# Performance work log

Measured on AMD Instinct MI355X. Metric: run time of the kernel, lower is better.

The kernel has to match this reference:

```python
import jax, jax.numpy as jnp
import numpy as np

HEADS = 4
DIM_HEAD = 128
DIM = 128
INNER = HEADS * DIM_HEAD  # 512
MAX_POS = 100
SCALE = DIM_HEAD ** -0.5


def setup_inputs() -> dict:
    key = jax.random.key(0)
    ks = jax.random.split(key, 8)
    b, h, w = 2, 48, 64
    fmap1 = jax.random.normal(ks[0], (b, DIM, h, w), jnp.float32)
    fmap2 = jax.random.normal(ks[1], (b, DIM, h, w), jnp.float32)
    Wqk = jax.random.normal(ks[2], (2 * INNER, DIM), jnp.float32) * 0.05
    Wv = jax.random.normal(ks[3], (INNER, DIM), jnp.float32) * 0.05
    rel_h = jax.random.normal(ks[4], (2 * MAX_POS - 1, DIM_HEAD), jnp.float32) * 0.05
    rel_w = jax.random.normal(ks[5], (2 * MAX_POS - 1, DIM_HEAD), jnp.float32) * 0.05
    Wp = jax.random.normal(ks[6], (DIM, INNER), jnp.float32) * 0.05
    gamma = jnp.full((1,), 0.1, jnp.float32)  # nonzero so the attn path is active
    return {"fmap1": fmap1, "fmap2": fmap2, "Wqk": Wqk, "Wv": Wv,
            "rel_h": rel_h, "rel_w": rel_w, "Wp": Wp, "gamma": gamma}


def _aggregate(fmap, Wqk, Wv, rel_h, rel_w, Wp, gamma):
    b, c, H, W = fmap.shape
    # 1x1 conv = channel matmul
    qk = jnp.einsum('oc,bchw->bohw', Wqk, fmap)
    q = qk[:, :INNER] * SCALE  # k chunk unused (position-only similarity)
    # b (n d) h w -> b n h w d
    q = q.reshape(b, HEADS, DIM_HEAD, H, W).transpose(0, 1, 3, 4, 2)
    v = jnp.einsum('oc,bchw->bohw', Wv, fmap)
    v = v.reshape(b, HEADS, DIM_HEAD, H, W).transpose(0, 1, 3, 4, 2).reshape(b, HEADS, H * W, DIM_HEAD)
    # relative position similarity (RelPosEmb)
    idx_h = jnp.arange(H)[:, None] - jnp.arange(H)[None, :] + (MAX_POS - 1)  # (H,H)
    idx_w = jnp.arange(W)[:, None] - jnp.arange(W)[None, :] + (MAX_POS - 1)  # (W,W)
    He = rel_h[idx_h]  # (x,u,d)
    We = rel_w[idx_w]  # (y,v,d)
    hs = jnp.einsum('bnxyd,xud->bnxyu', q, He)  # (b,n,x,y,u)
    ws = jnp.einsum('bnxyd,yvd->bnxyv', q, We)  # (b,n,x,y,v)
    sim = hs[..., :, None] + ws[..., None, :]   # (b,n,x,y,u,v)
    sim = sim.reshape(b, HEADS, H * W, H * W)
    attn = jax.nn.softmax(sim, axis=-1)
    out = jnp.einsum('bnij,bnjd->bnid', attn, v)  # (b,n,hw,d)
    out = out.reshape(b, HEADS, H, W, DIM_HEAD).transpose(0, 1, 4, 2, 3).reshape(b, INNER, H, W)
    out = jnp.einsum('oc,bchw->bohw', Wp, out)  # project (dim != inner_dim)
    return fmap + gamma[0] * out


def reference(fmap1, fmap2, Wqk, Wv, rel_h, rel_w, Wp, gamma):
    out1 = _aggregate(fmap1, Wqk, Wv, rel_h, rel_w, Wp, gamma)
    out2 = _aggregate(fmap2, Wqk, Wv, rel_h, rel_w, Wp, gamma)
    return (out1, out2)
```

## Files before the change

### kernel.cpp

```cpp
#include <hip/hip_runtime.h>
#include <cstdint>
#include <cstddef>

typedef short bf16x8 __attribute__((ext_vector_type(8)));
typedef float f32x4 __attribute__((ext_vector_type(4)));

#define HH 48
#define WW 64
#define HWSZ 3072
#define SCALE_Q 0.08838834764831845f

__device__ __forceinline__ float b2f(unsigned short u) {
    union { unsigned int i; float f; } c; c.i = ((unsigned int)u) << 16; return c.f;
}
__device__ __forceinline__ unsigned short f2b(float f) {
    union { float f; unsigned int i; } c; c.f = f;
    unsigned int r = (c.i + 0x7fffu + ((c.i >> 16) & 1u)) >> 16;
    return (unsigned short)r;
}

__global__ __launch_bounds__(256) void k_transpose(const float* __restrict__ f0,
                                                   const float* __restrict__ f1,
                                                   unsigned short* __restrict__ Xb) {
    __shared__ float t[32][33];
    int fb = blockIdx.z; int f = fb >> 1, bb = fb & 1;
    const float* src = f ? f1 : f0;
    int pT = blockIdx.x * 32, cT = blockIdx.y * 32;
    int tx = threadIdx.x, ty = threadIdx.y;
#pragma unroll
    for (int i = 0; i < 4; ++i) {
        int c = cT + ty + i * 8, pos = pT + tx;
        t[ty + i * 8][tx] = src[(size_t)(bb * 128 + c) * HWSZ + pos];
    }
    __syncthreads();
#pragma unroll
    for (int i = 0; i < 4; ++i) {
        int pos = pT + ty + i * 8, c = cT + tx;
        Xb[(size_t)(fb * HWSZ + pos) * 128 + c] = f2b(t[tx][ty + i * 8]);
    }
}

__global__ __launch_bounds__(256) void k_weights(const float* __restrict__ Wqk,
                                                 const float* __restrict__ Wv,
                                                 const float* __restrict__ Wp,
                                                 unsigned short* __restrict__ Wcat,
                                                 unsigned short* __restrict__ Wpb) {
    int idx = blockIdx.x * 256 + threadIdx.x;
    if (idx < 131072) {
        int o = idx >> 7, c = idx & 127;
        float v = (o < 512) ? Wqk[o * 128 + c] * SCALE_Q : Wv[(o - 512) * 128 + c];
        Wcat[idx] = f2b(v);
    } else {
        int j = idx - 131072;
        Wpb[j] = f2b(Wp[j]);
    }
}

__global__ __launch_bounds__(256) void k_qv(const unsigned short* __restrict__ Xb,
                                            const unsigned short* __restrict__ Wcat,
                                            unsigned short* __restrict__ Qx,
                                            unsigned short* __restrict__ Vt) {
    __shared__ unsigned short Asub[64 * 136];
    __shared__ unsigned short Bsub[128 * 136];
    int mt = blockIdx.x, nt = blockIdx.y, fb = blockIdx.z;
    int tid = threadIdx.x;
    const unsigned short* asrc = Xb + (size_t)(fb * HWSZ + mt * 64) * 128;
    const unsigned short* bsrc = Wcat + (size_t)nt * 128 * 128;
    for (int ch = tid; ch < 1024; ch += 256) {
        int row = ch >> 4, seg = ch & 15;
        *(bf16x8*)&Asub[row * 136 + seg * 8] = *(const bf16x8*)(asrc + ch * 8);
    }
    for (int ch = tid; ch < 2048; ch += 256) {
        int row = ch >> 4, seg = ch & 15;
        *(bf16x8*)&Bsub[row * 136 + seg * 8] = *(const bf16x8*)(bsrc + ch * 8);
    }
    __syncthreads();
    int l = tid & 63, w = tid >> 6;
    int wm = w >> 1, wn = w & 1;
    int lr = l & 15, lk8 = (l >> 4) * 8;
    f32x4 acc[2][4] = {};
#pragma unroll
    for (int kt = 0; kt < 4; ++kt) {
        bf16x8 a[2], b[4];
#pragma unroll
        for (int m = 0; m < 2; ++m)
            a[m] = *(const bf16x8*)&Asub[(wm * 32 + m * 16 + lr) * 136 + kt * 32 + lk8];
#pragma unroll
        for (int n = 0; n < 4; ++n)
            b[n] = *(const bf16x8*)&Bsub[(wn * 64 + n * 16 + lr) * 136 + kt * 32 + lk8];
#pragma unroll
        for (int m = 0; m < 2; ++m)
#pragma unroll
            for (int n = 0; n < 4; ++n)
                acc[m][n] = __builtin_amdgcn_mfma_f32_16x16x32_bf16(a[m], b[n], acc[m][n], 0, 0, 0);
    }
    int f = fb >> 1, bb = fb & 1;
#pragma unroll
    for (int m = 0; m < 2; ++m)
#pragma unroll
        for (int n = 0; n < 4; ++n) {
            int o = nt * 128 + wn * 64 + n * 16 + lr;
            int pos0 = mt * 64 + wm * 32 + m * 16 + (l >> 4) * 4;
            if (o < 512) {
                int nh = o >> 7, d = o & 127;
#pragma unroll
                for (int r = 0; r < 4; ++r) {
                    int pos = pos0 + r, x = pos >> 6, y = pos & 63;
                    Qx[(size_t)((f * 48 + x) * 512 + (bb * 4 + nh) * 64 + y) * 128 + d] = f2b(acc[m][n][r]);
                }
            } else {
                int oo = o - 512, nh = oo >> 7, d = oo & 127;
                uint2 val;
                val.x = (unsigned int)f2b(acc[m][n][0]) | ((unsigned int)f2b(acc[m][n][1]) << 16);
                val.y = (unsigned int)f2b(acc[m][n][2]) | ((unsigned int)f2b(acc[m][n][3]) << 16);
                *(uint2*)&Vt[(size_t)((fb * 4 + nh) * 128 + d) * HWSZ + pos0] = val;
            }
        }
}

__global__ __launch_bounds__(256) void k_ph(const unsigned short* __restrict__ Qx,
                                            const float* __restrict__ rel_h,
                                            unsigned short* __restrict__ PH) {
    __shared__ float sm[4][16][52];
    int x = blockIdx.x, f = blockIdx.y;
    int tid = threadIdx.x, l = tid & 63, w = tid >> 6;
    int lr = l & 15, lk8 = (l >> 4) * 8;
    bf16x8 bh[3][4];
#pragma unroll
    for (int ut = 0; ut < 3; ++ut) {
        int u = ut * 16 + lr, rr = x - u + 99;
#pragma unroll
        for (int kt = 0; kt < 4; ++kt) {
            const float* s = rel_h + rr * 128 + kt * 32 + lk8;
            float4 a0 = *(const float4*)s, a1 = *(const float4*)(s + 4);
            bf16x8 pk;
            pk[0] = (short)f2b(a0.x); pk[1] = (short)f2b(a0.y); pk[2] = (short)f2b(a0.z); pk[3] = (short)f2b(a0.w);
            pk[4] = (short)f2b(a1.x); pk[5] = (short)f2b(a1.y); pk[6] = (short)f2b(a1.z); pk[7] = (short)f2b(a1.w);
            bh[ut][kt] = pk;
        }
    }
    const unsigned short* qbase = Qx + (size_t)(f * 48 + x) * 512 * 128;
    unsigned short* phbase = PH + (size_t)(f * 48 + x) * 512 * 48;
    for (int mt = 0; mt < 8; ++mt) {
        int rg = w * 128 + mt * 16 + lr;
        const unsigned short* qrow = qbase + (size_t)rg * 128;
        bf16x8 a[4];
#pragma unroll
        for (int kt = 0; kt < 4; ++kt) a[kt] = *(const bf16x8*)(qrow + kt * 32 + lk8);
        f32x4 acc[3] = {};
#pragma unroll
        for (int kt = 0; kt < 4; ++kt)
#pragma unroll
            for (int ut = 0; ut < 3; ++ut)
                acc[ut] = __builtin_amdgcn_mfma_f32_16x16x32_bf16(a[kt], bh[ut][kt], acc[ut], 0, 0, 0);
        __syncthreads();
#pragma unroll
        for (int ut = 0; ut < 3; ++ut)
#pragma unroll
            for (int r = 0; r < 4; ++r)
                sm[w][(l >> 4) * 4 + r][ut * 16 + lr] = acc[ut][r];
        __syncthreads();
        int part = l >> 4;
        float vb[12];
        float mx = -1e30f;
#pragma unroll
        for (int j = 0; j < 12; ++j) { vb[j] = sm[w][lr][part * 12 + j]; mx = fmaxf(mx, vb[j]); }
        mx = fmaxf(mx, __shfl_xor(mx, 16, 64));
        mx = fmaxf(mx, __shfl_xor(mx, 32, 64));
        float ssum = 0.f;
#pragma unroll
        for (int j = 0; j < 12; ++j) { vb[j] = __expf(vb[j] - mx); ssum += vb[j]; }
        ssum += __shfl_xor(ssum, 16, 64);
        ssum += __shfl_xor(ssum, 32, 64);
        float inv = 1.0f / ssum;
        unsigned short* dst = phbase + (size_t)(w * 128 + mt * 16 + lr) * 48 + part * 12;
#pragma unroll
        for (int j = 0; j < 12; ++j) dst[j] = f2b(vb[j] * inv);
    }
}

__global__ __launch_bounds__(256) void k_pw(const unsigned short* __restrict__ Qx,
                                            const float* __restrict__ rel_w,
                                            unsigned short* __restrict__ PW) {
    __shared__ float sm[4][16][68];
    int y = blockIdx.x, f = blockIdx.y;
    int tid = threadIdx.x, l = tid & 63, w = tid >> 6;
    int lr = l & 15, lk8 = (l >> 4) * 8;
    bf16x8 bw[4][4];
#pragma unroll
    for (int vt = 0; vt < 4; ++vt) {
        int v = vt * 16 + lr, rr = y - v + 99;
#pragma unroll
        for (int kt = 0; kt < 4; ++kt) {
            const float* s = rel_w + rr * 128 + kt * 32 + lk8;
            float4 a0 = *(const float4*)s, a1 = *(const float4*)(s + 4);
            bf16x8 pk;
            pk[0] = (short)f2b(a0.x); pk[1] = (short)f2b(a0.y); pk[2] = (short)f2b(a0.z); pk[3] = (short)f2b(a0.w);
            pk[4] = (short)f2b(a1.x); pk[5] = (short)f2b(a1.y); pk[6] = (short)f2b(a1.z); pk[7] = (short)f2b(a1.w);
            bw[vt][kt] = pk;
        }
    }
    for (int mt = 0; mt < 6; ++mt) {
        int rg = w * 96 + mt * 16 + lr;
        int bn = rg / 48, xx = rg - bn * 48;
        const unsigned short* qrow = Qx + (size_t)((f * 48 + xx) * 512 + bn * 64 + y) * 128;
        bf16x8 a[4];
#pragma unroll
        for (int kt = 0; kt < 4; ++kt) a[kt] = *(const bf16x8*)(qrow + kt * 32 + lk8);
        f32x4 acc[4] = {};
#pragma unroll
        for (int kt = 0; kt < 4; ++kt)
#pragma unroll
            for (int vt = 0; vt < 4; ++vt)
                acc[vt] = __builtin_amdgcn_mfma_f32_16x16x32_bf16(a[kt], bw[vt][kt], acc[vt], 0, 0, 0);
        __syncthreads();
#pragma unroll
        for (int vt = 0; vt < 4; ++vt)
#pragma unroll
            for (int r = 0; r < 4; ++r)
                sm[w][(l >> 4) * 4 + r][vt * 16 + lr] = acc[vt][r];
        __syncthreads();
        int part = l >> 4;
        float vb[16];
        float mx = -1e30f;
#pragma unroll
        for (int j = 0; j < 16; ++j) { vb[j] = sm[w][lr][part * 16 + j]; mx = fmaxf(mx, vb[j]); }
        mx = fmaxf(mx, __shfl_xor(mx, 16, 64));
        mx = fmaxf(mx, __shfl_xor(mx, 32, 64));
        float ssum = 0.f;
#pragma unroll
        for (int j = 0; j < 16; ++j) { vb[j] = __expf(vb[j] - mx); ssum += vb[j]; }
        ssum += __shfl_xor(ssum, 16, 64);
        ssum += __shfl_xor(ssum, 32, 64);
        float inv = 1.0f / ssum;
        unsigned short* dst = PW + (size_t)((f * 64 + y) * 384 + rg) * 64 + part * 16;
#pragma unroll
        for (int j = 0; j < 16; ++j) dst[j] = f2b(vb[j] * inv);
    }
}

__global__ __launch_bounds__(256, 3) void k_attn(const unsigned short* __restrict__ PH,
                                                 const unsigned short* __restrict__ PW,
                                                 const unsigned short* __restrict__ Vt,
                                                 unsigned short* __restrict__ AO) {
    __shared__ unsigned short phl[48 * 128];
    __shared__ unsigned short vbuf[2][64 * 64];
    int bid = blockIdx.x;
    int r16 = bid & 15;
    int rest = bid >> 4;
    int t = rest >> 1, dh = rest & 1;
    int fbn = (r16 & 7) * 2 + (r16 >> 3);
    int f = fbn >> 3, bidx = (fbn >> 2) & 1, nh = fbn & 3;
    int fb = f * 2 + bidx, bn = bidx * 4 + nh;
    int tid = threadIdx.x;
    int l = tid & 63, wd = tid >> 6;
    int lr = l & 15, lg = l >> 4, lk8 = lg * 8;

    const unsigned short* vsrc = Vt + (size_t)((fb * 4 + nh) * 128 + dh * 64) * HWSZ;
    int sd = tid >> 2, sch = tid & 3;
    const unsigned short* vsrow0 = vsrc + (size_t)sd * HWSZ + sch * 8;
    const unsigned short* vsrow1 = vsrow0 + 32;
    int vdoff0 = sd * 64 + ((sch ^ (sd & 7)) * 8);
    int vdoff1 = sd * 64 + (((sch + 4) ^ (sd & 7)) * 8);

    bf16x8 r0a = *(const bf16x8*)(vsrow0);
    bf16x8 r0b = *(const bf16x8*)(vsrow1);

    for (int i = tid; i < 3072; i += 256) {
        int up2 = i >> 7, q = i & 127;
        int xy = t * 128 + q, x = xy >> 6, y = xy & 63;
        unsigned int wv = *(const unsigned int*)(PH + ((size_t)(f * 48 + x) * 512 + bn * 64 + y) * 48 + up2 * 2);
        int qoff = (q & 15) * 8 + (q >> 4);
        phl[(up2 * 2) * 128 + qoff]     = (unsigned short)(wv & 0xffffu);
        phl[(up2 * 2 + 1) * 128 + qoff] = (unsigned short)(wv >> 16);
    }
    bf16x8 b[8][2];
#pragma unroll
    for (int n = 0; n < 8; ++n) {
        int xy = t * 128 + n * 16 + lr;
        int x = xy >> 6, y = xy & 63;
        const unsigned short* pwr = PW + ((size_t)(f * 64 + y) * 384 + bn * 48 + x) * 64;
        b[n][0] = *(const bf16x8*)(pwr + lk8);
        b[n][1] = *(const bf16x8*)(pwr + 32 + lk8);
    }
    *(bf16x8*)&vbuf[0][vdoff0] = r0a;
    *(bf16x8*)&vbuf[0][vdoff1] = r0b;
    __syncthreads();

    int arow = wd * 16 + lr;
    int ao0 = arow * 64 + ((lg ^ (arow & 7)) * 8);
    int ao1 = arow * 64 + (((4 + lg) ^ (arow & 7)) * 8);
    const unsigned short* phrow = &phl[lr * 8];
    f32x4 acc[8] = {};
    const f32x4 zero4 = {0.f, 0.f, 0.f, 0.f};
    int cur = 0;
    for (int u = 0; u < 48; ++u) {
        bf16x8 ra, rb;
        if (u < 47) {
            ra = *(const bf16x8*)(vsrow0 + (size_t)(u + 1) * 64);
            rb = *(const bf16x8*)(vsrow1 + (size_t)(u + 1) * 64);
        }
        bf16x8 av0 = *(const bf16x8*)&vbuf[cur][ao0];
        bf16x8 av1 = *(const bf16x8*)&vbuf[cur][ao1];
        bf16x8 phv = *(const bf16x8*)(phrow + u * 128);
#pragma unroll
        for (int n = 0; n < 8; ++n) {
            f32x4 Y = __builtin_amdgcn_mfma_f32_16x16x32_bf16(av0, b[n][0], zero4, 0, 0, 0);
            Y = __builtin_amdgcn_mfma_f32_16x16x32_bf16(av1, b[n][1], Y, 0, 0, 0);
            float p = b2f((unsigned short)phv[n]);
            acc[n] += p * Y;
        }
        if (u < 47) {
            *(bf16x8*)&vbuf[cur ^ 1][vdoff0] = ra;
            *(bf16x8*)&vbuf[cur ^ 1][vdoff1] = rb;
        }
        __syncthreads();
        cur ^= 1;
    }
    unsigned short* aobase = AO + (size_t)fb * HWSZ * 512 + nh * 128 + dh * 64 + wd * 16 + lg * 4;
#pragma unroll
    for (int n = 0; n < 8; ++n) {
        int q = t * 128 + n * 16 + lr;
        uint2 val;
        val.x = (unsigned int)f2b(acc[n][0]) | ((unsigned int)f2b(acc[n][1]) << 16);
        val.y = (unsigned int)f2b(acc[n][2]) | ((unsigned int)f2b(acc[n][3]) << 16);
        *(uint2*)(aobase + (size_t)q * 512) = val;
    }
}

__global__ __launch_bounds__(256) void k_proj(const unsigned short* __restrict__ AO,
                                              const unsigned short* __restrict__ Wpb,
                                              const float* __restrict__ f0,
                                              const float* __restrict__ f1,
                                              const float* __restrict__ gamma,
                                              float* __restrict__ out) {
    __shared__ unsigned short Asub[64 * 136];
    __shared__ unsigned short Bsub[128 * 136];
    int t = blockIdx.x, fb = blockIdx.y;
    int f = fb >> 1, bb = fb & 1;
    int tid = threadIdx.x;
    int l = tid & 63, w = tid >> 6;
    int wm = w >> 1, wn = w & 1;
    int lr = l & 15, lk8 = (l >> 4) * 8;
    f32x4 acc[2][4] = {};
    for (int ks = 0; ks < 4; ++ks) {
        if (ks) __syncthreads();
        for (int ch = tid; ch < 1024; ch += 256) {
            int row = ch >> 4, seg = ch & 15;
            *(bf16x8*)&Asub[row * 136 + seg * 8] =
                *(const bf16x8*)(AO + (size_t)(fb * HWSZ + t * 64 + row) * 512 + ks * 128 + seg * 8);
        }
        for (int ch = tid; ch < 2048; ch += 256) {
            int row = ch >> 4, seg = ch & 15;
            *(bf16x8*)&Bsub[row * 136 + seg * 8] =
                *(const bf16x8*)(Wpb + (size_t)row * 512 + ks * 128 + seg * 8);
        }
        __syncthreads();
#pragma unroll
        for (int kt = 0; kt < 4; ++kt) {
            bf16x8 a[2], b[4];
#pragma unroll
            for (int m = 0; m < 2; ++m)
                a[m] = *(const bf16x8*)&Asub[(wm * 32 + m * 16 + lr) * 136 + kt * 32 + lk8];
#pragma unroll
            for (int n = 0; n < 4; ++n)
                b[n] = *(const bf16x8*)&Bsub[(wn * 64 + n * 16 + lr) * 136 + kt * 32 + lk8];
#pragma unroll
            for (int m = 0; m < 2; ++m)
#pragma unroll
                for (int n = 0; n < 4; ++n)
                    acc[m][n] = __builtin_amdgcn_mfma_f32_16x16x32_bf16(a[m], b[n], acc[m][n], 0, 0, 0);
        }
    }
    const float* fmapf = f ? f1 : f0;
    float g = gamma[0];
#pragma unroll
    for (int m = 0; m < 2; ++m)
#pragma unroll
        for (int n = 0; n < 4; ++n) {
            int c = wn * 64 + n * 16 + lr;
            int pos0 = t * 64 + wm * 32 + m * 16 + (l >> 4) * 4;
            size_t addr = (size_t)(bb * 128 + c) * HWSZ + pos0;
            float4 fv = *(const float4*)(fmapf + addr);
            float4 ov;
            ov.x = fv.x + g * acc[m][n][0];
            ov.y = fv.y + g * acc[m][n][1];
            ov.z = fv.z + g * acc[m][n][2];
            ov.w = fv.w + g * acc[m][n][3];
            *(float4*)(out + (size_t)f * 786432 + addr) = ov;
        }
}

extern "C" void kernel_launch(void* const* d_in, const int* in_sizes, int n_in,
                              void* d_out, int out_size, void* d_ws, size_t ws_size,
                              hipStream_t stream) {
    (void)in_sizes; (void)n_in; (void)out_size; (void)ws_size;
    const float* fmap1 = (const float*)d_in[0];
    const float* fmap2 = (const float*)d_in[1];
    const float* Wqk   = (const float*)d_in[2];
    const float* Wv    = (const float*)d_in[3];
    const float* rel_h = (const float*)d_in[4];
    const float* rel_w = (const float*)d_in[5];
    const float* Wp    = (const float*)d_in[6];
    const float* gamma = (const float*)d_in[7];
    float* out = (float*)d_out;
    char* ws = (char*)d_ws;

    unsigned short* Xb   = (unsigned short*)(ws + 0);
    unsigned short* Wcat = (unsigned short*)(ws + 3145728);
    unsigned short* Wpb  = (unsigned short*)(ws + 3407872);
    unsigned short* Qx   = (unsigned short*)(ws + 3538944);
    unsigned short* AO   = Qx;
    unsigned short* Vt   = (unsigned short*)(ws + 16121856);
    unsigned short* PH   = (unsigned short*)(ws + 28704768);
    unsigned short* PW   = (unsigned short*)(ws + 33423360);

    k_transpose<<<dim3(96, 4, 4), dim3(32, 8), 0, stream>>>(fmap1, fmap2, Xb);
    k_weights<<<dim3(768), dim3(256), 0, stream>>>(Wqk, Wv, Wp, Wcat, Wpb);
    k_qv<<<dim3(48, 8, 4), dim3(256), 0, stream>>>(Xb, Wcat, Qx, Vt);
    k_ph<<<dim3(48, 2), dim3(256), 0, stream>>>(Qx, rel_h, PH);
    k_pw<<<dim3(64, 2), dim3(256), 0, stream>>>(Qx, rel_w, PW);
    k_attn<<<dim3(768), dim3(256), 0, stream>>>(PH, PW, Vt, AO);
    k_proj<<<dim3(48, 4), dim3(256), 0, stream>>>(AO, Wpb, fmap1, fmap2, gamma, out);
}
```

Baseline: 118.3 us.

## Split softmax kernels over more blocks and deepen V prefetch in attention loop

k_ph and k_pw gain a z grid dimension, so each block handles two row tiles instead of all 6 or 8. This raises the block count from 96/128 to 384 to fill more compute units. k_attn now stages two u-slices of V per shared-memory buffer with a two-phase-ahead register prefetch, which halves the number of barriers. In exchange it uses more LDS and registers, which may reduce occupancy under launch_bounds(256,3), and the rel_h/rel_w tables are now reloaded by every split block.

After: 116.6 us. No clear change (-1.4%).

```diff
diff --git a/kernel.cpp b/kernel.cpp
--- a/kernel.cpp
+++ b/kernel.cpp
@@ -122,7 +122,7 @@
                                             const float* __restrict__ rel_h,
                                             unsigned short* __restrict__ PH) {
     __shared__ float sm[4][16][52];
-    int x = blockIdx.x, f = blockIdx.y;
+    int x = blockIdx.x, f = blockIdx.y, mtz = blockIdx.z;
     int tid = threadIdx.x, l = tid & 63, w = tid >> 6;
     int lr = l & 15, lk8 = (l >> 4) * 8;
     bf16x8 bh[3][4];
@@ -141,7 +141,7 @@
     }
     const unsigned short* qbase = Qx + (size_t)(f * 48 + x) * 512 * 128;
     unsigned short* phbase = PH + (size_t)(f * 48 + x) * 512 * 48;
-    for (int mt = 0; mt < 8; ++mt) {
+    for (int mt = mtz * 2; mt < mtz * 2 + 2; ++mt) {
         int rg = w * 128 + mt * 16 + lr;
         const unsigned short* qrow = qbase + (size_t)rg * 128;
         bf16x8 a[4];
@@ -183,7 +183,7 @@
                                             const float* __restrict__ rel_w,
                                             unsigned short* __restrict__ PW) {
     __shared__ float sm[4][16][68];
-    int y = blockIdx.x, f = blockIdx.y;
+    int y = blockIdx.x, f = blockIdx.y, mtz = blockIdx.z;
     int tid = threadIdx.x, l = tid & 63, w = tid >> 6;
     int lr = l & 15, lk8 = (l >> 4) * 8;
     bf16x8 bw[4][4];
@@ -200,7 +200,7 @@
             bw[vt][kt] = pk;
         }
     }
-    for (int mt = 0; mt < 6; ++mt) {
+    for (int mt = mtz * 2; mt < mtz * 2 + 2; ++mt) {
         int rg = w * 96 + mt * 16 + lr;
         int bn = rg / 48, xx = rg - bn * 48;
         const unsigned short* qrow = Qx + (size_t)((f * 48 + xx) * 512 + bn * 64 + y) * 128;
@@ -244,7 +244,7 @@
                                                  const unsigned short* __restrict__ Vt,
                                                  unsigned short* __restrict__ AO) {
     __shared__ unsigned short phl[48 * 128];
-    __shared__ unsigned short vbuf[2][64 * 64];
+    __shared__ unsigned short vbuf[2][2][64 * 64];
     int bid = blockIdx.x;
     int r16 = bid & 15;
     int rest = bid >> 4;
@@ -257,14 +257,20 @@
     int lr = l & 15, lg = l >> 4, lk8 = lg * 8;
 
     const unsigned short* vsrc = Vt + (size_t)((fb * 4 + nh) * 128 + dh * 64) * HWSZ;
-    int sd = tid >> 2, sch = tid & 3;
-    const unsigned short* vsrow0 = vsrc + (size_t)sd * HWSZ + sch * 8;
-    const unsigned short* vsrow1 = vsrow0 + 32;
-    int vdoff0 = sd * 64 + ((sch ^ (sd & 7)) * 8);
-    int vdoff1 = sd * 64 + (((sch + 4) ^ (sd & 7)) * 8);
-
-    bf16x8 r0a = *(const bf16x8*)(vsrow0);
-    bf16x8 r0b = *(const bf16x8*)(vsrow1);
+    int sd = tid >> 3, sch = tid & 7;
+    const unsigned short* vs0 = vsrc + (size_t)sd * HWSZ + sch * 8;
+    const unsigned short* vs1 = vs0 + (size_t)32 * HWSZ;
+    int wo0 = sd * 64 + ((sch ^ (sd & 7)) * 8);
+    int wo1 = wo0 + 32 * 64;
+
+    bf16x8 p0a = *(const bf16x8*)(vs0);
+    bf16x8 p0b = *(const bf16x8*)(vs1);
+    bf16x8 p1a = *(const bf16x8*)(vs0 + 64);
+    bf16x8 p1b = *(const bf16x8*)(vs1 + 64);
+    bf16x8 q0a = *(const bf16x8*)(vs0 + 128);
+    bf16x8 q0b = *(const bf16x8*)(vs1 + 128);
+    bf16x8 q1a = *(const bf16x8*)(vs0 + 192);
+    bf16x8 q1b = *(const bf16x8*)(vs1 + 192);
 
     for (int i = tid; i < 3072; i += 256) {
         int up2 = i >> 7, q = i & 127;
@@ -283,8 +289,10 @@
         b[n][0] = *(const bf16x8*)(pwr + lk8);
         b[n][1] = *(const bf16x8*)(pwr + 32 + lk8);
     }
-    *(bf16x8*)&vbuf[0][vdoff0] = r0a;
-    *(bf16x8*)&vbuf[0][vdoff1] = r0b;
+    *(bf16x8*)&vbuf[0][0][wo0] = p0a;
+    *(bf16x8*)&vbuf[0][0][wo1] = p0b;
+    *(bf16x8*)&vbuf[0][1][wo0] = p1a;
+    *(bf16x8*)&vbuf[0][1][wo1] = p1b;
     __syncthreads();
 
     int arow = wd * 16 + lr;
@@ -293,29 +301,39 @@
     const unsigned short* phrow = &phl[lr * 8];
     f32x4 acc[8] = {};
     const f32x4 zero4 = {0.f, 0.f, 0.f, 0.f};
-    int cur = 0;
-    for (int u = 0; u < 48; ++u) {
-        bf16x8 ra, rb;
-        if (u < 47) {
-            ra = *(const bf16x8*)(vsrow0 + (size_t)(u + 1) * 64);
-            rb = *(const bf16x8*)(vsrow1 + (size_t)(u + 1) * 64);
-        }
-        bf16x8 av0 = *(const bf16x8*)&vbuf[cur][ao0];
-        bf16x8 av1 = *(const bf16x8*)&vbuf[cur][ao1];
-        bf16x8 phv = *(const bf16x8*)(phrow + u * 128);
-#pragma unroll
-        for (int n = 0; n < 8; ++n) {
-            f32x4 Y = __builtin_amdgcn_mfma_f32_16x16x32_bf16(av0, b[n][0], zero4, 0, 0, 0);
-            Y = __builtin_amdgcn_mfma_f32_16x16x32_bf16(av1, b[n][1], Y, 0, 0, 0);
-            float p = b2f((unsigned short)phv[n]);
-            acc[n] += p * Y;
-        }
-        if (u < 47) {
-            *(bf16x8*)&vbuf[cur ^ 1][vdoff0] = ra;
-            *(bf16x8*)&vbuf[cur ^ 1][vdoff1] = rb;
-        }
-        __syncthreads();
-        cur ^= 1;
+    for (int ph = 0; ph < 24; ++ph) {
+        int cur = ph & 1;
+        bf16x8 n0a = q0a, n0b = q0b, n1a = q1a, n1b = q1b;
+        if (ph + 2 < 24) {
+            const unsigned short* s0 = vs0 + (size_t)(2 * ph + 4) * 64;
+            const unsigned short* s1 = vs1 + (size_t)(2 * ph + 4) * 64;
+            n0a = *(const bf16x8*)(s0);
+            n0b = *(const bf16x8*)(s1);
+            n1a = *(const bf16x8*)(s0 + 64);
+            n1b = *(const bf16x8*)(s1 + 64);
+        }
+        if (ph + 1 < 24) {
+            *(bf16x8*)&vbuf[cur ^ 1][0][wo0] = q0a;
+            *(bf16x8*)&vbuf[cur ^ 1][0][wo1] = q0b;
+            *(bf16x8*)&vbuf[cur ^ 1][1][wo0] = q1a;
+            *(bf16x8*)&vbuf[cur ^ 1][1][wo1] = q1b;
+        }
+#pragma unroll
+        for (int uu = 0; uu < 2; ++uu) {
+            int u = 2 * ph + uu;
+            bf16x8 av0 = *(const bf16x8*)&vbuf[cur][uu][ao0];
+            bf16x8 av1 = *(const bf16x8*)&vbuf[cur][uu][ao1];
+            bf16x8 phv = *(const bf16x8*)(phrow + u * 128);
+#pragma unroll
+            for (int n = 0; n < 8; ++n) {
+                f32x4 Y = __builtin_amdgcn_mfma_f32_16x16x32_bf16(av0, b[n][0], zero4, 0, 0, 0);
+                Y = __builtin_amdgcn_mfma_f32_16x16x32_bf16(av1, b[n][1], Y, 0, 0, 0);
+                float p = b2f((unsigned short)phv[n]);
+                acc[n] += p * Y;
+            }
+        }
+        __syncthreads();
+        q0a = n0a; q0b = n0b; q1a = n1a; q1b = n1b;
     }
     unsigned short* aobase = AO + (size_t)fb * HWSZ * 512 + nh * 128 + dh * 64 + wd * 16 + lg * 4;
 #pragma unroll
@@ -418,8 +436,8 @@
     k_transpose<<<dim3(96, 4, 4), dim3(32, 8), 0, stream>>>(fmap1, fmap2, Xb);
     k_weights<<<dim3(768), dim3(256), 0, stream>>>(Wqk, Wv, Wp, Wcat, Wpb);
     k_qv<<<dim3(48, 8, 4), dim3(256), 0, stream>>>(Xb, Wcat, Qx, Vt);
-    k_ph<<<dim3(48, 2), dim3(256), 0, stream>>>(Qx, rel_h, PH);
-    k_pw<<<dim3(64, 2), dim3(256), 0, stream>>>(Qx, rel_w, PW);
+    k_ph<<<dim3(48, 2, 4), dim3(256), 0, stream>>>(Qx, rel_h, PH);
+    k_pw<<<dim3(64, 2, 3), dim3(256), 0, stream>>>(Qx, rel_w, PW);
     k_attn<<<dim3(768), dim3(256), 0, stream>>>(PH, PW, Vt, AO);
     k_proj<<<dim3(48, 4), dim3(256), 0, stream>>>(AO, Wpb, fmap1, fmap2, gamma, out);
 }
```

## Relayout V per row so attention loads MFMA operands directly from global

Applied to the files above, without the earlier changes.

Changes the V layout written by the QV kernel to [head][u][d][v], so each attention wave can load its MFMA A-operands straight from global memory into registers. This removes the LDS double buffer and the per-iteration __syncthreads, using a three-deep register prefetch instead. Separately, the PH and PW softmax kernels get a z grid dimension that splits their row-tile loops, raising block count from 96/128 to 384. The attention change relies on global/L2 latency being hidden by register prefetch, and the split kernels redo the rel-embedding loads in every block.

Result: slower. 317.9 us (+168.9%).

```diff
diff --git a/kernel.cpp b/kernel.cpp
--- a/kernel.cpp
+++ b/kernel.cpp
@@ -110,10 +110,11 @@
                 }
             } else {
                 int oo = o - 512, nh = oo >> 7, d = oo & 127;
+                int u = pos0 >> 6, v = pos0 & 63;
                 uint2 val;
                 val.x = (unsigned int)f2b(acc[m][n][0]) | ((unsigned int)f2b(acc[m][n][1]) << 16);
                 val.y = (unsigned int)f2b(acc[m][n][2]) | ((unsigned int)f2b(acc[m][n][3]) << 16);
-                *(uint2*)&Vt[(size_t)((fb * 4 + nh) * 128 + d) * HWSZ + pos0] = val;
+                *(uint2*)&Vt[(((size_t)(fb * 4 + nh) * 48 + u) * 128 + d) * 64 + v] = val;
             }
         }
 }
@@ -122,7 +123,7 @@
                                             const float* __restrict__ rel_h,
                                             unsigned short* __restrict__ PH) {
     __shared__ float sm[4][16][52];
-    int x = blockIdx.x, f = blockIdx.y;
+    int x = blockIdx.x, f = blockIdx.y, mtz = blockIdx.z;
     int tid = threadIdx.x, l = tid & 63, w = tid >> 6;
     int lr = l & 15, lk8 = (l >> 4) * 8;
     bf16x8 bh[3][4];
@@ -141,7 +142,7 @@
     }
     const unsigned short* qbase = Qx + (size_t)(f * 48 + x) * 512 * 128;
     unsigned short* phbase = PH + (size_t)(f * 48 + x) * 512 * 48;
-    for (int mt = 0; mt < 8; ++mt) {
+    for (int mt = mtz * 2; mt < mtz * 2 + 2; ++mt) {
         int rg = w * 128 + mt * 16 + lr;
         const unsigned short* qrow = qbase + (size_t)rg * 128;
         bf16x8 a[4];
@@ -183,7 +184,7 @@
                                             const float* __restrict__ rel_w,
                                             unsigned short* __restrict__ PW) {
     __shared__ float sm[4][16][68];
-    int y = blockIdx.x, f = blockIdx.y;
+    int y = blockIdx.x, f = blockIdx.y, mtz = blockIdx.z;
     int tid = threadIdx.x, l = tid & 63, w = tid >> 6;
     int lr = l & 15, lk8 = (l >> 4) * 8;
     bf16x8 bw[4][4];
@@ -200,7 +201,7 @@
             bw[vt][kt] = pk;
         }
     }
-    for (int mt = 0; mt < 6; ++mt) {
+    for (int mt = mtz * 2; mt < mtz * 2 + 2; ++mt) {
         int rg = w * 96 + mt * 16 + lr;
         int bn = rg / 48, xx = rg - bn * 48;
         const unsigned short* qrow = Qx + (size_t)((f * 48 + xx) * 512 + bn * 64 + y) * 128;
@@ -244,7 +245,6 @@
                                                  const unsigned short* __restrict__ Vt,
                                                  unsigned short* __restrict__ AO) {
     __shared__ unsigned short phl[48 * 128];
-    __shared__ unsigned short vbuf[2][64 * 64];
     int bid = blockIdx.x;
     int r16 = bid & 15;
     int rest = bid >> 4;
@@ -256,16 +256,6 @@
     int l = tid & 63, wd = tid >> 6;
     int lr = l & 15, lg = l >> 4, lk8 = lg * 8;
 
-    const unsigned short* vsrc = Vt + (size_t)((fb * 4 + nh) * 128 + dh * 64) * HWSZ;
-    int sd = tid >> 2, sch = tid & 3;
-    const unsigned short* vsrow0 = vsrc + (size_t)sd * HWSZ + sch * 8;
-    const unsigned short* vsrow1 = vsrow0 + 32;
-    int vdoff0 = sd * 64 + ((sch ^ (sd & 7)) * 8);
-    int vdoff1 = sd * 64 + (((sch + 4) ^ (sd & 7)) * 8);
-
-    bf16x8 r0a = *(const bf16x8*)(vsrow0);
-    bf16x8 r0b = *(const bf16x8*)(vsrow1);
-
     for (int i = tid; i < 3072; i += 256) {
         int up2 = i >> 7, q = i & 127;
         int xy = t * 128 + q, x = xy >> 6, y = xy & 63;
@@ -283,40 +273,42 @@
         b[n][0] = *(const bf16x8*)(pwr + lk8);
         b[n][1] = *(const bf16x8*)(pwr + 32 + lk8);
     }
-    *(bf16x8*)&vbuf[0][vdoff0] = r0a;
-    *(bf16x8*)&vbuf[0][vdoff1] = r0b;
+    const unsigned short* vrow = Vt + (size_t)(fb * 4 + nh) * 48 * 128 * 64
+                                    + (size_t)(dh * 64 + wd * 16 + lr) * 64 + lg * 8;
+    bf16x8 A0a = *(const bf16x8*)(vrow);
+    bf16x8 A0b = *(const bf16x8*)(vrow + 32);
+    bf16x8 A1a = *(const bf16x8*)(vrow + 8192);
+    bf16x8 A1b = *(const bf16x8*)(vrow + 8192 + 32);
+    bf16x8 A2a = *(const bf16x8*)(vrow + 16384);
+    bf16x8 A2b = *(const bf16x8*)(vrow + 16384 + 32);
     __syncthreads();
 
-    int arow = wd * 16 + lr;
-    int ao0 = arow * 64 + ((lg ^ (arow & 7)) * 8);
-    int ao1 = arow * 64 + (((4 + lg) ^ (arow & 7)) * 8);
     const unsigned short* phrow = &phl[lr * 8];
     f32x4 acc[8] = {};
     const f32x4 zero4 = {0.f, 0.f, 0.f, 0.f};
-    int cur = 0;
-    for (int u = 0; u < 48; ++u) {
-        bf16x8 ra, rb;
-        if (u < 47) {
-            ra = *(const bf16x8*)(vsrow0 + (size_t)(u + 1) * 64);
-            rb = *(const bf16x8*)(vsrow1 + (size_t)(u + 1) * 64);
-        }
-        bf16x8 av0 = *(const bf16x8*)&vbuf[cur][ao0];
-        bf16x8 av1 = *(const bf16x8*)&vbuf[cur][ao1];
-        bf16x8 phv = *(const bf16x8*)(phrow + u * 128);
-#pragma unroll
-        for (int n = 0; n < 8; ++n) {
-            f32x4 Y = __builtin_amdgcn_mfma_f32_16x16x32_bf16(av0, b[n][0], zero4, 0, 0, 0);
-            Y = __builtin_amdgcn_mfma_f32_16x16x32_bf16(av1, b[n][1], Y, 0, 0, 0);
-            float p = b2f((unsigned short)phv[n]);
-            acc[n] += p * Y;
-        }
-        if (u < 47) {
-            *(bf16x8*)&vbuf[cur ^ 1][vdoff0] = ra;
-            *(bf16x8*)&vbuf[cur ^ 1][vdoff1] = rb;
-        }
-        __syncthreads();
-        cur ^= 1;
-    }
+
+#define STEP(U, Aa, Ab)                                                                     \
+    {                                                                                       \
+        bf16x8 phv = *(const bf16x8*)(phrow + (U) * 128);                                   \
+        _Pragma("unroll")                                                                   \
+        for (int n_ = 0; n_ < 8; ++n_) {                                                    \
+            f32x4 Y_ = __builtin_amdgcn_mfma_f32_16x16x32_bf16(Aa, b[n_][0], zero4, 0, 0, 0); \
+            Y_ = __builtin_amdgcn_mfma_f32_16x16x32_bf16(Ab, b[n_][1], Y_, 0, 0, 0);        \
+            acc[n_] += b2f((unsigned short)phv[n_]) * Y_;                                   \
+        }                                                                                   \
+        if ((U) + 3 < 48) {                                                                 \
+            Aa = *(const bf16x8*)(vrow + (size_t)((U) + 3) * 8192);                         \
+            Ab = *(const bf16x8*)(vrow + (size_t)((U) + 3) * 8192 + 32);                    \
+        }                                                                                   \
+    }
+
+    for (int uu = 0; uu < 48; uu += 3) {
+        STEP(uu + 0, A0a, A0b);
+        STEP(uu + 1, A1a, A1b);
+        STEP(uu + 2, A2a, A2b);
+    }
+#undef STEP
+
     unsigned short* aobase = AO + (size_t)fb * HWSZ * 512 + nh * 128 + dh * 64 + wd * 16 + lg * 4;
 #pragma unroll
     for (int n = 0; n < 8; ++n) {
@@ -418,8 +410,8 @@
     k_transpose<<<dim3(96, 4, 4), dim3(32, 8), 0, stream>>>(fmap1, fmap2, Xb);
     k_weights<<<dim3(768), dim3(256), 0, stream>>>(Wqk, Wv, Wp, Wcat, Wpb);
     k_qv<<<dim3(48, 8, 4), dim3(256), 0, stream>>>(Xb, Wcat, Qx, Vt);
-    k_ph<<<dim3(48, 2), dim3(256), 0, stream>>>(Qx, rel_h, PH);
-    k_pw<<<dim3(64, 2), dim3(256), 0, stream>>>(Qx, rel_w, PW);
+    k_ph<<<dim3(48, 2, 4), dim3(256), 0, stream>>>(Qx, rel_h, PH);
+    k_pw<<<dim3(64, 2, 3), dim3(256), 0, stream>>>(Qx, rel_w, PW);
     k_attn<<<dim3(768), dim3(256), 0, stream>>>(PH, PW, Vt, AO);
     k_proj<<<dim3(48, 4), dim3(256), 0, stream>>>(AO, Wpb, fmap1, fmap2, gamma, out);
 }
```
